# Kernel optimization log

Hardware: AMD Instinct MI355X
Metric: run time of the kernel (lower is better)

Reference implementation:

```python
import jax, jax.numpy as jnp
import numpy as np

THRESHOLD = 0.5
NEG_POS_RATIO = 3
ALPHA = 1.0
B, P, C, O = 64, 8732, 81, 32


def setup_inputs() -> dict:
    key = jax.random.key(0)
    k1, k2, k3, k4, k5, k6 = jax.random.split(key, 6)
    pred_locs = jax.random.normal(k1, (B, P, 4), dtype=jnp.float32)
    pred_scores = jax.random.normal(k2, (B, P, C), dtype=jnp.float32)
    # valid ground-truth corner boxes: sample center/size, convert to xy, clip to [0,1]
    ctr = jax.random.uniform(k3, (B, O, 2), minval=0.1, maxval=0.9)
    wh = jax.random.uniform(k4, (B, O, 2), minval=0.05, maxval=0.4)
    boxes = jnp.clip(jnp.concatenate([ctr - wh / 2, ctr + wh / 2], axis=-1), 0.0, 1.0)
    labels = jax.random.randint(k5, (B, O), 1, C, dtype=jnp.int64)
    pc = jax.random.uniform(k6, (P, 2), minval=0.05, maxval=0.95)
    pwh = jax.random.uniform(jax.random.fold_in(k6, 1), (P, 2), minval=0.05, maxval=0.3)
    priors_cxcy = jnp.concatenate([pc, pwh], axis=-1)
    return {"pred_locs": pred_locs, "pred_scores": pred_scores,
            "boxes": boxes, "labels": labels, "priors_cxcy": priors_cxcy}


def _jaccard(b, priors_xy):
    # b: [O,4] xy, priors_xy: [P,4] xy -> [O,P]
    lo = jnp.maximum(b[:, None, :2], priors_xy[None, :, :2])
    hi = jnp.minimum(b[:, None, 2:], priors_xy[None, :, 2:])
    inter = jnp.prod(jnp.clip(hi - lo, 0.0), axis=-1)
    area_b = jnp.prod(b[:, 2:] - b[:, :2], axis=-1)
    area_p = jnp.prod(priors_xy[:, 2:] - priors_xy[:, :2], axis=-1)
    return inter / (area_b[:, None] + area_p[None, :] - inter)


def _forward(pred_locs, pred_scores, boxes, labels, priors_cxcy):
    priors_xy = jnp.concatenate([priors_cxcy[:, :2] - priors_cxcy[:, 2:] / 2,
                                 priors_cxcy[:, :2] + priors_cxcy[:, 2:] / 2], axis=1)
    n_obj = boxes.shape[1]

    def match(b, l):
        ov = _jaccard(b, priors_xy)                      # [O,P]
        ov_fp = jnp.max(ov, axis=0)                      # [P]
        obj_fp = jnp.argmax(ov, axis=0)                  # [P]
        prior_fo = jnp.argmax(ov, axis=1)                # [O]
        obj_fp = obj_fp.at[prior_fo].set(jnp.arange(n_obj))
        ov_fp = ov_fp.at[prior_fo].set(1.0)
        lab = jnp.where(ov_fp < THRESHOLD, 0, l[obj_fp]) # [P]
        pt = b[obj_fp]                                   # [P,4] xy
        c = jnp.concatenate([(pt[:, 2:] + pt[:, :2]) / 2, pt[:, 2:] - pt[:, :2]], axis=1)
        g = jnp.concatenate([(c[:, :2] - priors_cxcy[:, :2]) / (priors_cxcy[:, 2:] / 10),
                             jnp.log(c[:, 2:] / priors_cxcy[:, 2:]) * 5], axis=1)
        return g, lab

    true_locs, true_classes = jax.vmap(match)(boxes, labels)  # [B,P,4], [B,P]

    pos = true_classes != 0                                   # [B,P]
    n_pos = jnp.sum(pos, axis=1)                              # [B]
    n_pos_total = jnp.sum(n_pos).astype(pred_locs.dtype)

    # L1Loss (mean over positive elements, 4 coords each)
    loc_abs = jnp.abs(pred_locs - true_locs) * pos[..., None].astype(pred_locs.dtype)
    loc_loss = jnp.sum(loc_abs) / (n_pos_total * 4.0)

    # per-prior cross entropy
    logp = jax.nn.log_softmax(pred_scores, axis=-1)           # [B,P,C]
    ce = -jnp.take_along_axis(logp, true_classes[..., None], axis=-1)[..., 0]  # [B,P]

    posf = pos.astype(ce.dtype)
    conf_pos_sum = jnp.sum(ce * posf)
    conf_neg = jnp.where(pos, 0.0, ce)
    conf_neg_sorted = -jnp.sort(-conf_neg, axis=1)            # descending
    ranks = jnp.arange(ce.shape[1])[None, :]
    hard = ranks < (NEG_POS_RATIO * n_pos)[:, None]
    conf_hard_neg_sum = jnp.sum(conf_neg_sorted * hard.astype(ce.dtype))

    conf_loss = (conf_hard_neg_sum + conf_pos_sum) / n_pos_total
    return conf_loss + ALPHA * loc_loss


def reference(pred_locs, pred_scores, boxes, labels, priors_cxcy):
    return _forward(pred_locs, pred_scores, boxes, labels, priors_cxcy)
```

## Files before the change

### kernel.cpp

```cpp
#include <hip/hip_runtime.h>

#define BB 64
#define PP 8732
#define OO 32
#define CC 81
#define NEGPOS 3
#define NCH_B 32
#define CHB 273
#define NCEB 137

#define WS_BESTP  0
#define WS_CENEG  (WS_BESTP + BB*NCH_B*OO*8)
#define WS_CEPOS  (WS_CENEG + BB*PP*4)
#define WS_LSUMB  (WS_CEPOS + BB*NCEB*4)
#define WS_NPOSB  (WS_LSUMB + BB*NCEB*4)
#define WS_HARDB  (WS_NPOSB + BB*NCEB*4)
#define WS_DONE   (WS_HARDB + BB*4)

__global__ __launch_bounds__(512) void match_obj(
    const float* __restrict__ boxes, const float* __restrict__ priors,
    unsigned long long* __restrict__ bestp, int* __restrict__ done)
{
    const int b = blockIdx.y, ch = blockIdx.x, tid = threadIdx.x;
    __shared__ float sbx[OO * 4];
    __shared__ unsigned long long sred[8 * OO];
    if (tid < OO * 4) sbx[tid] = boxes[b * OO * 4 + tid];
    if (ch == 0 && b == 0 && tid == 0) *done = 0;
    __syncthreads();

    const int o = tid & 31, sub = tid >> 5;
    const float b0 = sbx[o*4+0], b1 = sbx[o*4+1], b2 = sbx[o*4+2], b3 = sbx[o*4+3];
    const float barea = (b2 - b0) * (b3 - b1);
    const int base = ch * CHB;
    unsigned long long best = 0ull;
    for (int i = sub; i < CHB; i += 16) {
        int p = base + i;
        if (p >= PP) break;
        float4 pr = ((const float4*)priors)[p];
        float plx = pr.x - pr.z * 0.5f, ply = pr.y - pr.w * 0.5f;
        float phx = pr.x + pr.z * 0.5f, phy = pr.y + pr.w * 0.5f;
        float parea = pr.z * pr.w;
        float lox = fmaxf(b0, plx), loy = fmaxf(b1, ply);
        float hix = fminf(b2, phx), hiy = fminf(b3, phy);
        float inter = fmaxf(hix - lox, 0.0f) * fmaxf(hiy - loy, 0.0f);
        float iou = inter / (barea + parea - inter);
        unsigned long long enc =
            ((unsigned long long)__float_as_uint(iou) << 32) | (unsigned)(~(unsigned)p);
        best = (enc > best) ? enc : best;
    }
    unsigned long long w = __shfl_down(best, 32, 64);
    best = (w > best) ? w : best;
    const int wid = tid >> 6, lane = tid & 63;
    if (lane < 32) sred[wid * OO + o] = best;
    __syncthreads();
    if (tid < OO) {
        unsigned long long m = 0ull;
#pragma unroll
        for (int wv = 0; wv < 8; ++wv) {
            unsigned long long v = sred[wv * OO + tid];
            m = (v > m) ? v : m;
        }
        bestp[(b * NCH_B + ch) * OO + tid] = m;
    }
}

__global__ __launch_bounds__(256) void ce_match(
    const float* __restrict__ scores, const float* __restrict__ pred_locs,
    const float* __restrict__ boxes, const int* __restrict__ labels,
    const float* __restrict__ priors,
    const unsigned long long* __restrict__ bestp,
    float* __restrict__ ce_neg, float* __restrict__ cepos,
    float* __restrict__ lsum_bc, int* __restrict__ npos_bc)
{
    const int b = blockIdx.y, ch = blockIdx.x, tid = threadIdx.x;
    const int base = ch * 64;
    __shared__ float sbx[OO * 4];
    __shared__ int   slab[OO];
    __shared__ int   spfo[OO];
    __shared__ float srf[4], srl[4];
    __shared__ int   sri[4];

    if (tid < OO * 4) sbx[tid] = boxes[b * OO * 4 + tid];
    if (tid >= 224)   slab[tid - 224] = labels[b * OO + (tid - 224)];
    if (tid < OO) {
        unsigned long long m = 0ull;
#pragma unroll 4
        for (int c = 0; c < NCH_B; ++c) {
            unsigned long long v = bestp[(b * NCH_B + c) * OO + tid];
            m = (v > m) ? v : m;
        }
        spfo[tid] = (int)(~(unsigned)(m & 0xFFFFFFFFull));
    }
    __syncthreads();

    const int g = tid >> 2, j = tid & 3;
    const int p = base + g;
    float posc = 0.0f, lsum = 0.0f; int lpos = 0;

    if (p < PP) {
        const long long bp = (long long)b * PP + p;
        const float* __restrict__ v = scores + bp * CC;

        float d[21];
#pragma unroll
        for (int k = 0; k < 5; ++k) {
            const int c4 = (4 * k + j) * 4;
#pragma unroll
            for (int q = 0; q < 4; ++q) d[4*k+q] = v[c4 + q];
        }
        d[20] = (j == 0) ? v[80] : -3.0e38f;

        float4 pr = ((const float4*)priors)[p];
        float plx = pr.x - pr.z * 0.5f, ply = pr.y - pr.w * 0.5f;
        float phx = pr.x + pr.z * 0.5f, phy = pr.y + pr.w * 0.5f;
        float parea = pr.z * pr.w;
        unsigned long long eb = 0ull;
#pragma unroll
        for (int k = 0; k < 8; ++k) {
            const int oo = j * 8 + k;
            float c0 = sbx[oo*4+0], c1 = sbx[oo*4+1], c2 = sbx[oo*4+2], c3 = sbx[oo*4+3];
            float lox = fmaxf(c0, plx), loy = fmaxf(c1, ply);
            float hix = fminf(c2, phx), hiy = fminf(c3, phy);
            float inter = fmaxf(hix - lox, 0.0f) * fmaxf(hiy - loy, 0.0f);
            float iou = inter / ((c2 - c0) * (c3 - c1) + parea - inter);
            unsigned long long enc =
                ((unsigned long long)__float_as_uint(iou) << 32) | (unsigned)(~(unsigned)oo);
            eb = (enc > eb) ? enc : eb;
        }
        {
            unsigned long long t = __shfl_xor(eb, 1, 64); eb = (t > eb) ? t : eb;
            t = __shfl_xor(eb, 2, 64);                    eb = (t > eb) ? t : eb;
        }
        int o = (int)(~(unsigned)(eb & 0xFFFFFFFFull));
        float ov = __uint_as_float((unsigned)(eb >> 32));

#pragma unroll
        for (int oo = 0; oo < OO; ++oo)
            if (spfo[oo] == p) { o = oo; ov = 1.0f; }
        const int l = (ov < 0.5f) ? 0 : slab[o];

        float m = d[20];
#pragma unroll
        for (int i = 0; i < 20; ++i) m = fmaxf(m, d[i]);
        m = fmaxf(m, __shfl_xor(m, 1, 64));
        m = fmaxf(m, __shfl_xor(m, 2, 64));

        float s = 0.0f;
#pragma unroll
        for (int i = 0; i < 21; ++i) s += __expf(d[i] - m);

        float vl = 0.0f;
        if (l == 80) { if (j == 0) vl = d[20]; }
        else { int c = l >> 2; if ((c & 3) == j) vl = d[4 * (c >> 2) + (l & 3)]; }

        s  += __shfl_xor(s, 1, 64);   s  += __shfl_xor(s, 2, 64);
        vl += __shfl_xor(vl, 1, 64);  vl += __shfl_xor(vl, 2, 64);

        float ce = m + __logf(s) - vl;
        if (j == 0) {
            ce_neg[bp] = (l != 0) ? 0.0f : ce;
            if (l != 0) {
                posc = ce; lpos = 1;
                float b0 = sbx[o*4+0], b1 = sbx[o*4+1], b2 = sbx[o*4+2], b3 = sbx[o*4+3];
                float gx = ((b0 + b2) * 0.5f - pr.x) / (pr.z * 0.1f);
                float gy = ((b1 + b3) * 0.5f - pr.y) / (pr.w * 0.1f);
                float gw = logf((b2 - b0) / pr.z) * 5.0f;
                float gh = logf((b3 - b1) / pr.w) * 5.0f;
                float4 pl = ((const float4*)pred_locs)[bp];
                lsum = fabsf(pl.x - gx) + fabsf(pl.y - gy)
                     + fabsf(pl.z - gw) + fabsf(pl.w - gh);
            }
        }
    }

    for (int off = 32; off > 0; off >>= 1) {
        posc += __shfl_down(posc, off, 64);
        lsum += __shfl_down(lsum, off, 64);
        lpos += __shfl_down(lpos, off, 64);
    }
    if ((tid & 63) == 0) { int w = tid >> 6; srf[w] = posc; srl[w] = lsum; sri[w] = lpos; }
    __syncthreads();
    if (tid == 0) {
        cepos[b * NCEB + ch]   = srf[0] + srf[1] + srf[2] + srf[3];
        lsum_bc[b * NCEB + ch] = srl[0] + srl[1] + srl[2] + srl[3];
        npos_bc[b * NCEB + ch] = sri[0] + sri[1] + sri[2] + sri[3];
    }
}

__global__ __launch_bounds__(512) void topk_kernel(
    const float* __restrict__ ce_neg, const int* __restrict__ npos_bc,
    const float* __restrict__ cepos, const float* __restrict__ lsum_bc,
    float* __restrict__ hard_b, int* __restrict__ done, float* __restrict__ out)
{
    __shared__ float sv[PP];
    __shared__ int hist[256 * 16];
    __shared__ int ssum[256];
    __shared__ unsigned sel[2];
    __shared__ float sr[8];
    __shared__ int sKred[8];
    const int b = blockIdx.x, tid = threadIdx.x;
    for (int p = tid; p < PP; p += 512) sv[p] = ce_neg[b * PP + p];

    {
        int n = 0;
        for (int c = tid; c < NCEB; c += 512) n += npos_bc[b * NCEB + c];
        for (int off = 32; off > 0; off >>= 1) n += __shfl_down(n, off, 64);
        if ((tid & 63) == 0) sKred[tid >> 6] = n;
    }
    __syncthreads();
    int K;
    {
        int n = 0;
#pragma unroll
        for (int w = 0; w < 8; ++w) n += sKred[w];
        K = NEGPOS * n;
        if (K > PP) K = PP;
    }

    float hard = 0.0f;
    if (K > 0) {
        unsigned prefix = 0, mask = 0;
        unsigned remaining = (unsigned)K;
        for (int pass = 0; pass < 4; ++pass) {
            const int shift = 24 - 8 * pass;
            for (int i = tid; i < 256 * 16; i += 512) hist[i] = 0;
            __syncthreads();
            for (int p = tid; p < PP; p += 512) {
                unsigned u = __float_as_uint(sv[p]);
                if ((u & mask) == prefix)
                    atomicAdd(&hist[(((u >> shift) & 255) << 4) | (tid & 15)], 1);
            }
            __syncthreads();
            if (tid < 256) {
                int s = 0;
#pragma unroll
                for (int w = 0; w < 16; ++w) s += hist[(tid << 4) | w];
                ssum[tid] = s;
            }
            __syncthreads();
            for (int off = 1; off < 256; off <<= 1) {
                int vv = 0;
                if (tid < 256) vv = (tid + off < 256) ? ssum[tid + off] : 0;
                __syncthreads();
                if (tid < 256) ssum[tid] += vv;
                __syncthreads();
            }
            if (tid < 256 && (unsigned)ssum[tid] >= remaining &&
                (tid == 255 || (unsigned)ssum[tid + 1] < remaining)) {
                sel[0] = (unsigned)tid;
                sel[1] = remaining - ((tid == 255) ? 0u : (unsigned)ssum[tid + 1]);
            }
            __syncthreads();
            prefix |= sel[0] << shift;
            mask |= 0xFFu << shift;
            remaining = sel[1];
            __syncthreads();
        }
        float sgt = 0.0f;
        for (int p = tid; p < PP; p += 512) {
            unsigned u = __float_as_uint(sv[p]);
            if (u > prefix) sgt += sv[p];
        }
        for (int off = 32; off > 0; off >>= 1) sgt += __shfl_down(sgt, off, 64);
        if ((tid & 63) == 0) sr[tid >> 6] = sgt;
        __syncthreads();
        if (tid == 0) {
            hard = 0.0f;
#pragma unroll
            for (int w = 0; w < 8; ++w) hard += sr[w];
            hard += __uint_as_float(prefix) * (float)remaining;
        }
    }
    __shared__ int sticket;
    if (tid == 0) {
        hard_b[b] = hard;
        __threadfence();
        sticket = atomicAdd(done, 1);
    }
    __syncthreads();
    if (sticket != BB - 1) return;

    float cpos = 0.0f, labs = 0.0f, chard = 0.0f; int n = 0;
    for (int i = tid; i < BB * NCEB; i += 512) {
        cpos += cepos[i];
        labs += lsum_bc[i];
        n    += npos_bc[i];
    }
    if (tid < BB) chard = atomicAdd(&hard_b[tid], 0.0f);
    for (int off = 32; off > 0; off >>= 1) {
        cpos  += __shfl_down(cpos, off, 64);
        labs  += __shfl_down(labs, off, 64);
        chard += __shfl_down(chard, off, 64);
        n     += __shfl_down(n, off, 64);
    }
    __shared__ float f0[8], f1[8], f2[8];
    __shared__ int i3[8];
    if ((tid & 63) == 0) { int w = tid >> 6; f0[w] = cpos; f1[w] = labs; f2[w] = chard; i3[w] = n; }
    __syncthreads();
    if (tid == 0) {
        float a = 0.0f, bs = 0.0f, c = 0.0f; int nt = 0;
#pragma unroll
        for (int w = 0; w < 8; ++w) { a += f0[w]; bs += f1[w]; c += f2[w]; nt += i3[w]; }
        float nf = (float)nt;
        out[0] = (c + a) / nf + bs / (nf * 4.0f);
    }
}

extern "C" void kernel_launch(void* const* d_in, const int* in_sizes, int n_in,
                              void* d_out, int out_size, void* d_ws, size_t ws_size,
                              hipStream_t stream) {
    const float* pred_locs   = (const float*)d_in[0];
    const float* pred_scores = (const float*)d_in[1];
    const float* boxes       = (const float*)d_in[2];
    const int*   labels      = (const int*)d_in[3];
    const float* priors      = (const float*)d_in[4];
    float* out = (float*)d_out;

    char* ws = (char*)d_ws;
    unsigned long long* bestp = (unsigned long long*)(ws + WS_BESTP);
    float* ce_neg  = (float*)(ws + WS_CENEG);
    float* cepos   = (float*)(ws + WS_CEPOS);
    float* lsum_bc = (float*)(ws + WS_LSUMB);
    int*   nposbc  = (int*)(ws + WS_NPOSB);
    float* hard_b  = (float*)(ws + WS_HARDB);
    int*   done    = (int*)(ws + WS_DONE);

    match_obj<<<dim3(NCH_B, BB), 512, 0, stream>>>(boxes, priors, bestp, done);
    ce_match<<<dim3(NCEB, BB), 256, 0, stream>>>(pred_scores, pred_locs, boxes, labels,
                                                 priors, bestp,
                                                 ce_neg, cepos, lsum_bc, nposbc);
    topk_kernel<<<BB, 512, 0, stream>>>(ce_neg, nposbc, cepos, lsum_bc, hard_b, done, out);
}
```

Before: 303.8 us.

## Replace 4-pass 8-bit radix select with 3-pass 12/10/10-bit select

```diff
diff --git a/kernel.cpp b/kernel.cpp
--- a/kernel.cpp
+++ b/kernel.cpp
@@ -187,20 +187,50 @@
     }
 }
 
+__device__ __forceinline__ void suffix_select(
+    int* hist, int nbins, unsigned rem, unsigned* sel, int* wred, int tid)
+{
+    const int nb = nbins >> 9;
+    const int base = tid * nb;
+    int tot = 0;
+    for (int i = 0; i < nb; ++i) tot += hist[base + i];
+    const int lane = tid & 63, w = tid >> 6;
+    int s = tot;
+#pragma unroll
+    for (int off = 1; off < 64; off <<= 1) {
+        int v = __shfl_down(s, off, 64);
+        if (lane + off < 64) s += v;
+    }
+    if (lane == 0) wred[w] = s;
+    __syncthreads();
+    int after = s - tot;
+    for (int ww = w + 1; ww < 8; ++ww) after += wred[ww];
+    int cum = after;
+    for (int i = nb - 1; i >= 0; --i) {
+        int h = hist[base + i];
+        if ((unsigned)cum < rem && (unsigned)(cum + h) >= rem) {
+            sel[0] = (unsigned)(base + i);
+            sel[1] = rem - (unsigned)cum;
+        }
+        cum += h;
+    }
+    __syncthreads();
+}
+
 __global__ __launch_bounds__(512) void topk_kernel(
     const float* __restrict__ ce_neg, const int* __restrict__ npos_bc,
     const float* __restrict__ cepos, const float* __restrict__ lsum_bc,
     float* __restrict__ hard_b, int* __restrict__ done, float* __restrict__ out)
 {
     __shared__ float sv[PP];
-    __shared__ int hist[256 * 16];
-    __shared__ int ssum[256];
+    __shared__ int hist[4096];
+    __shared__ int wred[8];
     __shared__ unsigned sel[2];
     __shared__ float sr[8];
     __shared__ int sKred[8];
     const int b = blockIdx.x, tid = threadIdx.x;
-    for (int p = tid; p < PP; p += 512) sv[p] = ce_neg[b * PP + p];
-
+
+    for (int i = tid; i < 4096; i += 512) hist[i] = 0;
     {
         int n = 0;
         for (int c = tid; c < NCEB; c += 512) n += npos_bc[b * NCEB + c];
@@ -208,6 +238,12 @@
         if ((tid & 63) == 0) sKred[tid >> 6] = n;
     }
     __syncthreads();
+
+    for (int p = tid; p < PP; p += 512) {
+        float v = ce_neg[b * PP + p];
+        sv[p] = v;
+        atomicAdd(&hist[__float_as_uint(v) >> 20], 1);
+    }
     int K;
     {
         int n = 0;
@@ -216,46 +252,35 @@
         K = NEGPOS * n;
         if (K > PP) K = PP;
     }
+    __syncthreads();
 
     float hard = 0.0f;
     if (K > 0) {
-        unsigned prefix = 0, mask = 0;
-        unsigned remaining = (unsigned)K;
-        for (int pass = 0; pass < 4; ++pass) {
-            const int shift = 24 - 8 * pass;
-            for (int i = tid; i < 256 * 16; i += 512) hist[i] = 0;
-            __syncthreads();
-            for (int p = tid; p < PP; p += 512) {
-                unsigned u = __float_as_uint(sv[p]);
-                if ((u & mask) == prefix)
-                    atomicAdd(&hist[(((u >> shift) & 255) << 4) | (tid & 15)], 1);
-            }
-            __syncthreads();
-            if (tid < 256) {
-                int s = 0;
-#pragma unroll
-                for (int w = 0; w < 16; ++w) s += hist[(tid << 4) | w];
-                ssum[tid] = s;
-            }
-            __syncthreads();
-            for (int off = 1; off < 256; off <<= 1) {
-                int vv = 0;
-                if (tid < 256) vv = (tid + off < 256) ? ssum[tid + off] : 0;
-                __syncthreads();
-                if (tid < 256) ssum[tid] += vv;
-                __syncthreads();
-            }
-            if (tid < 256 && (unsigned)ssum[tid] >= remaining &&
-                (tid == 255 || (unsigned)ssum[tid + 1] < remaining)) {
-                sel[0] = (unsigned)tid;
-                sel[1] = remaining - ((tid == 255) ? 0u : (unsigned)ssum[tid + 1]);
-            }
-            __syncthreads();
-            prefix |= sel[0] << shift;
-            mask |= 0xFFu << shift;
-            remaining = sel[1];
-            __syncthreads();
-        }
+        suffix_select(hist, 4096, (unsigned)K, sel, wred, tid);
+        const unsigned b1 = sel[0], rem1 = sel[1];
+
+        for (int i = tid; i < 1024; i += 512) hist[i] = 0;
+        __syncthreads();
+        for (int p = tid; p < PP; p += 512) {
+            unsigned u = __float_as_uint(sv[p]);
+            if ((u >> 20) == b1) atomicAdd(&hist[(u >> 10) & 1023], 1);
+        }
+        __syncthreads();
+        suffix_select(hist, 1024, rem1, sel, wred, tid);
+        const unsigned b2 = sel[0], rem2 = sel[1];
+        const unsigned pre2 = (b1 << 20) | (b2 << 10);
+
+        for (int i = tid; i < 1024; i += 512) hist[i] = 0;
+        __syncthreads();
+        for (int p = tid; p < PP; p += 512) {
+            unsigned u = __float_as_uint(sv[p]);
+            if ((u >> 10) == (pre2 >> 10)) atomicAdd(&hist[u & 1023], 1);
+        }
+        __syncthreads();
+        suffix_select(hist, 1024, rem2, sel, wred, tid);
+        const unsigned prefix = pre2 | sel[0];
+        const unsigned remaining = sel[1];
+
         float sgt = 0.0f;
         for (int p = tid; p < PP; p += 512) {
             unsigned u = __float_as_uint(sv[p]);
```

Result: no change. 305.5 us (+0.6%).
